# Optimization experiments

Measured on AMD Instinct MI355X. Metric: run time of the kernel, lower is better.

The kernel has to match this reference:

```python
import jax, jax.numpy as jnp
import numpy as np

EPS = 1e-12  # torch F.normalize default eps


def _l2norm(x):
    return x / jnp.maximum(jnp.linalg.norm(x, axis=-1, keepdims=True), EPS)


def setup_inputs() -> dict:
    key = jax.random.key(0)
    k1, k2, k3, k4 = jax.random.split(key, 4)
    B, N, F = 2048, 128, 256
    drug = jax.random.normal(k1, (B, N, F), dtype=jnp.float32)
    cell = jax.random.normal(k2, (B, F), dtype=jnp.float32)
    # xavier_uniform bound for square [F,F]: sqrt(6/(F+F))
    bound = float(np.sqrt(6.0 / (F + F)))
    k = jax.random.uniform(k3, (F, F), minval=-bound, maxval=bound, dtype=jnp.float32)
    q = jax.random.uniform(k4, (F, F), minval=-bound, maxval=bound, dtype=jnp.float32)
    return {"drug": drug, "cell": cell, "k": k, "q": q}


def reference(drug, cell, k, q):
    d = _l2norm(drug)                 # [B, N, F]
    c = _l2norm(cell[:, None, :])     # [B, 1, F]
    drug_ = d @ k                     # [B, N, F]
    cell_ = c @ q                     # [B, 1, F]
    scores = jnp.einsum('bof,bnf->bon', cell_, drug_)  # [B, 1, N]
    attn = jax.nn.softmax(scores, axis=2)
    sim = jnp.einsum('bof,bnf->bon', c, d)             # [B, 1, N]
    return (attn * sim)[:, 0, :]      # [B, N]
```

## Files before the change

### kernel.cpp

```cpp
#include <hip/hip_runtime.h>
#include <math.h>

#define F 256
#define NROW 128
#define EPS 1e-12f

typedef float vf4 __attribute__((ext_vector_type(4)));

__global__ __launch_bounds__(256) void qkT_kernel(const float* __restrict__ q,
                                                  const float* __restrict__ k,
                                                  float* __restrict__ M) {
    __shared__ float qs[F];
    int f = blockIdx.x;
    qs[threadIdx.x] = q[(size_t)f * F + threadIdx.x];
    __syncthreads();
    int g = threadIdx.x;
    const float4* kr = (const float4*)(k + (size_t)g * F);
    const float4* qr = (const float4*)qs;
    float acc = 0.f;
#pragma unroll 8
    for (int j = 0; j < F / 4; j++) {
        float4 kv = kr[j];
        float4 qv = qr[j];
        acc += kv.x * qv.x + kv.y * qv.y + kv.z * qv.z + kv.w * qv.w;
    }
    M[(size_t)f * F + g] = acc;
}

__global__ __launch_bounds__(256) void fused_main(const float* __restrict__ drug,
                                                  const float* __restrict__ cell,
                                                  const float* __restrict__ M,
                                                  float* __restrict__ out) {
    int b = blockIdx.x;
    int tid = threadIdx.x;
    int wave = tid >> 6;
    int lane = tid & 63;
    int grp = lane >> 4;
    int l16 = lane & 15;

    __shared__ float sc[NROW];
    __shared__ float sm[NROW];
    __shared__ float red[4];
    __shared__ float wp[4][F];
    __shared__ float wsh[F];

    const float* crow = cell + (size_t)b * F;

    {
        int c = lane;
        int fp = wave;
        vf4 acc = {0.f, 0.f, 0.f, 0.f};
        const float* Mp = M + (size_t)(fp * 64) * F + 4 * c;
        const float* cp = crow + fp * 64;
#pragma unroll 8
        for (int f = 0; f < 64; f++) {
            vf4 m4 = *(const vf4*)(Mp + (size_t)f * F);
            float cf = cp[f];
            acc.x += cf * m4.x;
            acc.y += cf * m4.y;
            acc.z += cf * m4.z;
            acc.w += cf * m4.w;
        }
        *(vf4*)&wp[fp][4 * c] = acc;
    }
    __syncthreads();
    wsh[tid] = wp[0][tid] + wp[1][tid] + wp[2][tid] + wp[3][tid];

    vf4 c4[4];
    float cs = 0.f;
#pragma unroll
    for (int j = 0; j < 4; j++) {
        c4[j] = *(const vf4*)&crow[j * 64 + l16 * 4];
        cs += c4[j].x * c4[j].x + c4[j].y * c4[j].y + c4[j].z * c4[j].z + c4[j].w * c4[j].w;
    }
#pragma unroll
    for (int m = 1; m < 16; m <<= 1) cs += __shfl_xor(cs, m, 64);
    float invc = 1.0f / fmaxf(sqrtf(cs), EPS);
    __syncthreads();

    vf4 w4[4];
#pragma unroll
    for (int j = 0; j < 4; j++) w4[j] = *(const vf4*)&wsh[j * 64 + l16 * 4];

    const float* dbase = drug + (size_t)b * NROW * F;
#pragma unroll 2
    for (int it = 0; it < 8; it++) {
        int n = wave * 32 + it * 4 + grp;
        const float* drow = dbase + (size_t)n * F;
        float an = 0.f, aw = 0.f, ac = 0.f;
#pragma unroll
        for (int j = 0; j < 4; j++) {
            vf4 v = __builtin_nontemporal_load((const vf4*)&drow[j * 64 + l16 * 4]);
            an += v.x * v.x + v.y * v.y + v.z * v.z + v.w * v.w;
            aw += v.x * w4[j].x + v.y * w4[j].y + v.z * w4[j].z + v.w * w4[j].w;
            ac += v.x * c4[j].x + v.y * c4[j].y + v.z * c4[j].z + v.w * c4[j].w;
        }
#pragma unroll
        for (int m = 1; m < 16; m <<= 1) {
            an += __shfl_xor(an, m, 64);
            aw += __shfl_xor(aw, m, 64);
            ac += __shfl_xor(ac, m, 64);
        }
        if (l16 == 0) {
            float inv = invc / fmaxf(sqrtf(an), EPS);
            sc[n] = aw * inv;
            sm[n] = ac * inv;
        }
    }
    __syncthreads();

    float s = sc[tid & 127];
    float v = s;
#pragma unroll
    for (int m = 1; m < 64; m <<= 1) v = fmaxf(v, __shfl_xor(v, m, 64));
    if (lane == 0) red[wave] = v;
    __syncthreads();
    float gmax = fmaxf(fmaxf(red[0], red[1]), fmaxf(red[2], red[3]));
    float e = expf(s - gmax);
    float t = (tid < NROW) ? e : 0.f;
#pragma unroll
    for (int m = 1; m < 64; m <<= 1) t += __shfl_xor(t, m, 64);
    __syncthreads();
    if (lane == 0) red[wave] = t;
    __syncthreads();
    float tot = red[0] + red[1] + red[2] + red[3];
    if (tid < NROW) {
        out[(size_t)b * NROW + tid] = (e / tot) * sm[tid & 127];
    }
}

extern "C" void kernel_launch(void* const* d_in, const int* in_sizes, int n_in,
                              void* d_out, int out_size, void* d_ws, size_t ws_size,
                              hipStream_t stream) {
    const float* drug = (const float*)d_in[0];
    const float* cell = (const float*)d_in[1];
    const float* k = (const float*)d_in[2];
    const float* q = (const float*)d_in[3];
    float* out = (float*)d_out;

    int B = in_sizes[1] / F;

    float* M = (float*)d_ws;

    qkT_kernel<<<dim3(F), dim3(256), 0, stream>>>(q, k, M);
    fused_main<<<dim3(B), dim3(256), 0, stream>>>(drug, cell, M, out);
}
```

Before: 363.0 us.

## Process four batches per block to reuse M loads across batches

Each block now handles four batch rows instead of one. The 256x256 M matrix is read once per block and applied to four cell vectors, which cuts redundant M traffic. The softmax is reworked so each wave handles one batch with a single-wave reduction, removing the cross-wave shared-memory syncs. The cost is a quarter as many blocks (512) on a large GPU, more shared memory and registers per block, and a loop over four batches in series that may lower memory-level parallelism for streaming the drug tensor. The kernel also assumes B is divisible by 4.

```diff
diff --git a/kernel.cpp b/kernel.cpp
--- a/kernel.cpp
+++ b/kernel.cpp
@@ -3,6 +3,7 @@
 
 #define F 256
 #define NROW 128
+#define BPB 4
 #define EPS 1e-12f
 
 typedef float vf4 __attribute__((ext_vector_type(4)));
@@ -31,101 +32,108 @@
                                                   const float* __restrict__ cell,
                                                   const float* __restrict__ M,
                                                   float* __restrict__ out) {
-    int b = blockIdx.x;
+    int b0 = blockIdx.x * BPB;
     int tid = threadIdx.x;
     int wave = tid >> 6;
     int lane = tid & 63;
     int grp = lane >> 4;
     int l16 = lane & 15;
 
-    __shared__ float sc[NROW];
-    __shared__ float sm[NROW];
-    __shared__ float red[4];
-    __shared__ float wp[4][F];
-    __shared__ float wsh[F];
-
-    const float* crow = cell + (size_t)b * F;
+    __shared__ float wp[4][BPB][F];
+    __shared__ float wsh[BPB][F];
+    __shared__ float sc[BPB][NROW];
+    __shared__ float sm[BPB][NROW];
+    __shared__ float invc_sh[BPB];
 
     {
-        int c = lane;
-        int fp = wave;
-        vf4 acc = {0.f, 0.f, 0.f, 0.f};
-        const float* Mp = M + (size_t)(fp * 64) * F + 4 * c;
-        const float* cp = crow + fp * 64;
+        const float* Mp = M + (size_t)(wave * 64) * F + 4 * lane;
+        const float* cp = cell + (size_t)b0 * F + wave * 64;
+        vf4 acc[BPB];
+#pragma unroll
+        for (int bi = 0; bi < BPB; bi++) acc[bi] = (vf4){0.f, 0.f, 0.f, 0.f};
 #pragma unroll 8
         for (int f = 0; f < 64; f++) {
             vf4 m4 = *(const vf4*)(Mp + (size_t)f * F);
-            float cf = cp[f];
-            acc.x += cf * m4.x;
-            acc.y += cf * m4.y;
-            acc.z += cf * m4.z;
-            acc.w += cf * m4.w;
+#pragma unroll
+            for (int bi = 0; bi < BPB; bi++) {
+                float cf = cp[(size_t)bi * F + f];
+                acc[bi].x += cf * m4.x;
+                acc[bi].y += cf * m4.y;
+                acc[bi].z += cf * m4.z;
+                acc[bi].w += cf * m4.w;
+            }
         }
-        *(vf4*)&wp[fp][4 * c] = acc;
+#pragma unroll
+        for (int bi = 0; bi < BPB; bi++) *(vf4*)&wp[wave][bi][4 * lane] = acc[bi];
+    }
+    {
+        vf4 cv = *(const vf4*)&cell[(size_t)(b0 + wave) * F + 4 * lane];
+        float cs = cv.x * cv.x + cv.y * cv.y + cv.z * cv.z + cv.w * cv.w;
+#pragma unroll
+        for (int m = 1; m < 64; m <<= 1) cs += __shfl_xor(cs, m, 64);
+        if (lane == 0) invc_sh[wave] = 1.0f / fmaxf(sqrtf(cs), EPS);
     }
     __syncthreads();
-    wsh[tid] = wp[0][tid] + wp[1][tid] + wp[2][tid] + wp[3][tid];
-
-    vf4 c4[4];
-    float cs = 0.f;
 #pragma unroll
-    for (int j = 0; j < 4; j++) {
-        c4[j] = *(const vf4*)&crow[j * 64 + l16 * 4];
-        cs += c4[j].x * c4[j].x + c4[j].y * c4[j].y + c4[j].z * c4[j].z + c4[j].w * c4[j].w;
+    for (int bi = 0; bi < BPB; bi++) {
+        wsh[bi][tid] = wp[0][bi][tid] + wp[1][bi][tid] + wp[2][bi][tid] + wp[3][bi][tid];
     }
-#pragma unroll
-    for (int m = 1; m < 16; m <<= 1) cs += __shfl_xor(cs, m, 64);
-    float invc = 1.0f / fmaxf(sqrtf(cs), EPS);
     __syncthreads();
 
-    vf4 w4[4];
 #pragma unroll
-    for (int j = 0; j < 4; j++) w4[j] = *(const vf4*)&wsh[j * 64 + l16 * 4];
-
-    const float* dbase = drug + (size_t)b * NROW * F;
-#pragma unroll 2
-    for (int it = 0; it < 8; it++) {
-        int n = wave * 32 + it * 4 + grp;
-        const float* drow = dbase + (size_t)n * F;
-        float an = 0.f, aw = 0.f, ac = 0.f;
+    for (int bi = 0; bi < BPB; bi++) {
+        int b = b0 + bi;
+        vf4 w4[4], c4[4];
 #pragma unroll
         for (int j = 0; j < 4; j++) {
-            vf4 v = __builtin_nontemporal_load((const vf4*)&drow[j * 64 + l16 * 4]);
-            an += v.x * v.x + v.y * v.y + v.z * v.z + v.w * v.w;
-            aw += v.x * w4[j].x + v.y * w4[j].y + v.z * w4[j].z + v.w * w4[j].w;
-            ac += v.x * c4[j].x + v.y * c4[j].y + v.z * c4[j].z + v.w * c4[j].w;
+            w4[j] = *(const vf4*)&wsh[bi][j * 64 + l16 * 4];
+            c4[j] = *(const vf4*)&cell[(size_t)b * F + j * 64 + l16 * 4];
         }
+        float invc = invc_sh[bi];
+        const float* dbase = drug + (size_t)b * NROW * F;
+#pragma unroll 2
+        for (int it = 0; it < 8; it++) {
+            int n = wave * 32 + it * 4 + grp;
+            const float* drow = dbase + (size_t)n * F;
+            float an = 0.f, aw = 0.f, ac = 0.f;
 #pragma unroll
-        for (int m = 1; m < 16; m <<= 1) {
-            an += __shfl_xor(an, m, 64);
-            aw += __shfl_xor(aw, m, 64);
-            ac += __shfl_xor(ac, m, 64);
-        }
-        if (l16 == 0) {
-            float inv = invc / fmaxf(sqrtf(an), EPS);
-            sc[n] = aw * inv;
-            sm[n] = ac * inv;
+            for (int j = 0; j < 4; j++) {
+                vf4 v = __builtin_nontemporal_load((const vf4*)&drow[j * 64 + l16 * 4]);
+                an += v.x * v.x + v.y * v.y + v.z * v.z + v.w * v.w;
+                aw += v.x * w4[j].x + v.y * w4[j].y + v.z * w4[j].z + v.w * w4[j].w;
+                ac += v.x * c4[j].x + v.y * c4[j].y + v.z * c4[j].z + v.w * c4[j].w;
+            }
+#pragma unroll
+            for (int m = 1; m < 16; m <<= 1) {
+                an += __shfl_xor(an, m, 64);
+                aw += __shfl_xor(aw, m, 64);
+                ac += __shfl_xor(ac, m, 64);
+            }
+            if (l16 == 0) {
+                float inv = invc / fmaxf(sqrtf(an), EPS);
+                sc[bi][n] = aw * inv;
+                sm[bi][n] = ac * inv;
+            }
         }
     }
     __syncthreads();
 
-    float s = sc[tid & 127];
-    float v = s;
+    {
+        int bi = wave;
+        float s0 = sc[bi][lane];
+        float s1 = sc[bi][lane + 64];
+        float mx = fmaxf(s0, s1);
 #pragma unroll
-    for (int m = 1; m < 64; m <<= 1) v = fmaxf(v, __shfl_xor(v, m, 64));
-    if (lane == 0) red[wave] = v;
-    __syncthreads();
-    float gmax = fmaxf(fmaxf(red[0], red[1]), fmaxf(red[2], red[3]));
-    float e = expf(s - gmax);
-    float t = (tid < NROW) ? e : 0.f;
+        for (int m = 1; m < 64; m <<= 1) mx = fmaxf(mx, __shfl_xor(mx, m, 64));
+        float e0 = expf(s0 - mx);
+        float e1 = expf(s1 - mx);
+        float t = e0 + e1;
 #pragma unroll
-    for (int m = 1; m < 64; m <<= 1) t += __shfl_xor(t, m, 64);
-    __syncthreads();
-    if (lane == 0) red[wave] = t;
-    __syncthreads();
-    float tot = red[0] + red[1] + red[2] + red[3];
-    if (tid < NROW) {
-        out[(size_t)b * NROW + tid] = (e / tot) * sm[tid & 127];
+        for (int m = 1; m < 64; m <<= 1) t += __shfl_xor(t, m, 64);
+        float rt = 1.0f / t;
+        float* orow = out + (size_t)(b0 + bi) * NROW;
+        orow[lane] = e0 * rt * sm[bi][lane];
+        orow[lane + 64] = e1 * rt * sm[bi][lane + 64];
     }
 }
 
@@ -143,5 +151,5 @@
     float* M = (float*)d_ws;
 
     qkT_kernel<<<dim3(F), dim3(256), 0, stream>>>(q, k, M);
-    fused_main<<<dim3(B), dim3(256), 0, stream>>>(drug, cell, M, out);
+    fused_main<<<dim3(B / BPB), dim3(256), 0, stream>>>(drug, cell, M, out);
 }
```

Result: no change. 358.2 us (-1.3%).
